# Performance work log

Hardware: AMD Instinct MI355X
Metric: run time of the kernel (lower is better)

## Reference

```python
import jax, jax.numpy as jnp
import numpy as np

C = 512
GROUPS = 32
EPS = 1e-6


def group_norm(x, w, b):
    # x: [B, C, H, W]
    B, Cc, H, W = x.shape
    xg = x.reshape(B, GROUPS, Cc // GROUPS, H, W)
    mean = xg.mean(axis=(2, 3, 4), keepdims=True)
    var = xg.var(axis=(2, 3, 4), keepdims=True)
    xg = (xg - mean) * jax.lax.rsqrt(var + EPS)
    x = xg.reshape(B, Cc, H, W)
    return x * w[None, :, None, None] + b[None, :, None, None]


def conv1x1(x, w, b):
    # 1x1 conv == per-pixel channel matmul; w: [Cout, Cin]
    return jnp.einsum('bchw,oc->bohw', x, w) + b[None, :, None, None]


def setup_inputs() -> dict:
    key = jax.random.key(0)
    ks = jax.random.split(key, 11)
    s = 1.0 / np.sqrt(C)
    d = {
        'x': jax.random.normal(ks[0], (2, C, 64, 64), dtype=jnp.float32),
        'gn_w': jnp.ones((C,), jnp.float32),
        'gn_b': jnp.zeros((C,), jnp.float32),
        'wq': jax.random.normal(ks[1], (C, C), jnp.float32) * s,
        'bq': jax.random.normal(ks[2], (C,), jnp.float32) * 0.01,
        'wk': jax.random.normal(ks[3], (C, C), jnp.float32) * s,
        'bk': jax.random.normal(ks[4], (C,), jnp.float32) * 0.01,
        'wv': jax.random.normal(ks[5], (C, C), jnp.float32) * s,
        'bv': jax.random.normal(ks[6], (C,), jnp.float32) * 0.01,
        'wo': jax.random.normal(ks[7], (C, C), jnp.float32) * s,
        'bo': jax.random.normal(ks[8], (C,), jnp.float32) * 0.01,
    }
    return d


def reference(x, gn_w, gn_b, wq, bq, wk, bk, wv, bv, wo, bo):
    B, Cc, H, W = x.shape
    h = group_norm(x, gn_w, gn_b)
    q = conv1x1(h, wq, bq)  # [B,C,H,W]
    k = conv1x1(h, wk, bk)
    v = conv1x1(h, wv, bv)
    N = H * W
    q = q.reshape(B, Cc, N).transpose(0, 2, 1)   # b n c
    k = k.reshape(B, Cc, N)                      # b c n
    v = v.reshape(B, Cc, N)                      # b c n
    attn = jnp.einsum('bic,bcj->bij', q, k) * (Cc ** -0.5)  # [B,N,N]
    attn = jax.nn.softmax(attn, axis=-1)
    # h_[b,c,i] = sum_j v[b,c,j] * attn[b,i,j]
    h_ = jnp.einsum('bcj,bij->bci', v, attn).reshape(B, Cc, H, W)
    h_ = conv1x1(h_, wo, bo)
    return x + h_
```

## Files before the change

kernel.cpp:

```cpp
#include <hip/hip_runtime.h>


typedef __attribute__((ext_vector_type(8))) short bf16x8;
typedef __attribute__((ext_vector_type(4))) float f32x4;
typedef unsigned short u16;
typedef unsigned int u32;

__device__ __forceinline__ u16 f2bf(float f) {
  u32 u = __builtin_bit_cast(u32, f);
  return (u16)((u + 0x7FFFu + ((u >> 16) & 1u)) >> 16);
}
__device__ __forceinline__ float bf2f(u16 u) {
  return __builtin_bit_cast(float, (u32)u << 16);
}
__device__ __forceinline__ void gll16(const void* g, void* l) {
  __builtin_amdgcn_global_load_lds((const __attribute__((address_space(1))) u32*)g,
                                   (__attribute__((address_space(3))) u32*)l, 16, 0, 0);
}

__global__ __launch_bounds__(256) void gn_stats(const float* __restrict__ x,
                                                float* __restrict__ stats) {
  int bg = blockIdx.x >> 3, slice = blockIdx.x & 7;
  const float4* xp = (const float4*)(x + (size_t)bg * 65536 + slice * 8192);
  int t = threadIdx.x;
  float s = 0.f, ss = 0.f;
  for (int i = t; i < 2048; i += 256) {
    float4 v = xp[i];
    s += v.x + v.y + v.z + v.w;
    ss += v.x * v.x + v.y * v.y + v.z * v.z + v.w * v.w;
  }
  for (int off = 32; off > 0; off >>= 1) {
    s += __shfl_down(s, off);
    ss += __shfl_down(ss, off);
  }
  __shared__ float rs[4], rss[4];
  if ((t & 63) == 0) { rs[t >> 6] = s; rss[t >> 6] = ss; }
  __syncthreads();
  if (t == 0) {
    atomicAdd(&stats[bg * 2 + 0], rs[0] + rs[1] + rs[2] + rs[3]);
    atomicAdd(&stats[bg * 2 + 1], rss[0] + rss[1] + rss[2] + rss[3]);
  }
}

__global__ __launch_bounds__(256) void gn_apply(
    const float* __restrict__ x, const float* __restrict__ w,
    const float* __restrict__ b, const float* __restrict__ stats,
    u16* __restrict__ ht) {
  int bg = blockIdx.x >> 3, slice = blockIdx.x & 7;
  int batch = bg >> 5, g = bg & 31;
  const float* xp = x + (size_t)bg * 65536;
  float mean = stats[bg * 2 + 0] * (1.f / 65536.f);
  float var = stats[bg * 2 + 1] * (1.f / 65536.f) - mean * mean;
  float rstd = rsqrtf(var + 1e-6f);
  float wsc[16], bsc[16];
#pragma unroll
  for (int cc = 0; cc < 16; ++cc) {
    float wv = w[g * 16 + cc];
    wsc[cc] = wv * rstd;
    bsc[cc] = b[g * 16 + cc] - mean * wsc[cc];
  }
  u16* hp = ht + (size_t)batch * 4096 * 512 + g * 16;
  int t = threadIdx.x;
  for (int n = slice * 512 + t; n < slice * 512 + 512; n += 256) {
    union { u16 pk[16]; uint4 v4[2]; } u;
#pragma unroll
    for (int cc = 0; cc < 16; ++cc)
      u.pk[cc] = f2bf(xp[cc * 4096 + n] * wsc[cc] + bsc[cc]);
    uint4* dst = (uint4*)(hp + (size_t)n * 512);
    dst[0] = u.v4[0];
    dst[1] = u.v4[1];
  }
}

__global__ __launch_bounds__(256) void wcvt_kernel(
    const float* __restrict__ wq, const float* __restrict__ wk,
    const float* __restrict__ wv, const float* __restrict__ wo,
    const float* __restrict__ bq, const float* __restrict__ bk,
    u16* __restrict__ Wqk, u16* __restrict__ Wv, u16* __restrict__ Wo,
    float* __restrict__ Bqk, float* __restrict__ stats) {
  int i = blockIdx.x * 256 + threadIdx.x;
  Wqk[i] = f2bf(wq[i]);
  Wqk[262144 + i] = f2bf(wk[i]);
  Wv[i] = f2bf(wv[i]);
  Wo[i] = f2bf(wo[i]);
  if (i < 512) { Bqk[i] = bq[i]; Bqk[512 + i] = bk[i]; }
  if (blockIdx.x == 0 && threadIdx.x < 128) stats[threadIdx.x] = 0.f;
}

template <int BM, int BN, int MODE>
__global__ __launch_bounds__(256) void mfma_gemm(
    const u16* __restrict__ A, int sA, const u16* __restrict__ B, int sB,
    int K, const float* __restrict__ bias, const float* __restrict__ res,
    void* __restrict__ out, int ostr, float scale,
    u16* __restrict__ p1, u16* __restrict__ p2, u16* __restrict__ p3,
    size_t zsA, size_t zsB, size_t zsO) {
  constexpr int TM = BM / 32, TN = BN / 32;
  constexpr int SIA = BM / 32, SIB = BN / 32;
  __shared__ char sm[(BM + BN) * 128];
  char* As = sm;
  char* Bs = sm + BM * 128;
  int t = threadIdx.x;
  int w = t >> 6, lane = t & 63, quad = lane >> 4, ln = lane & 15;
  int wm = w >> 1, wn = w & 1;
  int m0 = blockIdx.y * BM, n0 = blockIdx.x * BN;
  int zb, ksplit;
  if (MODE == 5) { zb = blockIdx.z >> 2; ksplit = blockIdx.z & 3; }
  else           { zb = blockIdx.z;      ksplit = 0; }
  const u16* Ab = A + (size_t)zb * zsA;
  const u16* Bb = B + (size_t)zb * zsB;
  int kbase = ksplit * K;
  f32x4 acc[TM][TN] = {};

  for (int k0 = 0; k0 < K; k0 += 64) {
#pragma unroll
    for (int si = 0; si < SIA; ++si) {
      int s = (w * SIA + si) * 64 + lane;
      gll16(Ab + (size_t)(m0 + (s & (BM - 1))) * sA + kbase + k0 + (s / BM) * 8,
            As + (w * SIA + si) * 1024);
    }
#pragma unroll
    for (int si = 0; si < SIB; ++si) {
      int s = (w * SIB + si) * 64 + lane;
      gll16(Bb + (size_t)(n0 + (s & (BN - 1))) * sB + kbase + k0 + (s / BN) * 8,
            Bs + (w * SIB + si) * 1024);
    }
    __syncthreads();
#pragma unroll
    for (int ks = 0; ks < 2; ++ks) {
      bf16x8 af[TM], bfr[TN];
#pragma unroll
      for (int tm = 0; tm < TM; ++tm)
        af[tm] = *(const bf16x8*)(As + (((ks * 4 + quad) * BM) + wm * (BM / 2) + tm * 16 + ln) * 16);
#pragma unroll
      for (int tn = 0; tn < TN; ++tn)
        bfr[tn] = *(const bf16x8*)(Bs + (((ks * 4 + quad) * BN) + wn * (BN / 2) + tn * 16 + ln) * 16);
#pragma unroll
      for (int tm = 0; tm < TM; ++tm)
#pragma unroll
        for (int tn = 0; tn < TN; ++tn)
          acc[tm][tn] = __builtin_amdgcn_mfma_f32_16x16x32_bf16(af[tm], bfr[tn], acc[tm][tn], 0, 0, 0);
    }
    __syncthreads();
  }

  u16* pdst = nullptr;
  if (MODE == 5) {
    pdst = (ksplit == 0) ? (u16*)out : (ksplit == 1) ? p1
         : (ksplit == 2) ? p2 : p3;
    pdst += (size_t)zb * zsO;
  } else if (MODE != 2) {
    pdst = (u16*)out + (size_t)zb * zsO;
  }

#pragma unroll
  for (int tm = 0; tm < TM; ++tm) {
    int mb = m0 + wm * (BM / 2) + tm * 16 + quad * 4;
#pragma unroll
    for (int tn = 0; tn < TN; ++tn) {
      int n = n0 + wn * (BN / 2) + tn * 16 + ln;
      float bn = (MODE == 0) ? bias[n] : 0.f;
#pragma unroll
      for (int r = 0; r < 4; ++r) {
        int m = mb + r;
        float v = acc[tm][tn][r];
        if (MODE == 0) {
          pdst[(size_t)m * ostr + n] = f2bf(v + bn);
        } else if (MODE == 1) {
          pdst[(size_t)m * ostr + n] = f2bf(v + bias[m]);
        } else if (MODE == 2) {
          int bb = n >> 12, nn = n & 4095;
          size_t off = ((size_t)(bb * 512 + m)) * 4096 + nn;
          ((float*)out)[off] = v + bias[m] + res[off];
        } else if (MODE == 3) {
          pdst[(size_t)m * ostr + n] = f2bf(v * scale);
        } else {
          pdst[(size_t)m * ostr + n] = f2bf(v);
        }
      }
    }
  }
}

__global__ __launch_bounds__(256) void softmax_kernel(u16* __restrict__ S) {
  u16* sp = S + (size_t)blockIdx.x * 4096;
  int t = threadIdx.x;
  int w = t >> 6;
  uint4 a = ((const uint4*)sp)[t * 2];
  uint4 b = ((const uint4*)sp)[t * 2 + 1];
  u32 words[8] = {a.x, a.y, a.z, a.w, b.x, b.y, b.z, b.w};
  float v[16];
#pragma unroll
  for (int i = 0; i < 8; ++i) {
    v[2 * i] = bf2f((u16)(words[i] & 0xFFFF));
    v[2 * i + 1] = bf2f((u16)(words[i] >> 16));
  }
  float mx = v[0];
#pragma unroll
  for (int i = 1; i < 16; ++i) mx = fmaxf(mx, v[i]);
#pragma unroll
  for (int d = 1; d < 64; d <<= 1) mx = fmaxf(mx, __shfl_xor(mx, d));
  __shared__ float red[8];
  if ((t & 63) == 0) red[w] = mx;
  __syncthreads();
  mx = fmaxf(fmaxf(red[0], red[1]), fmaxf(red[2], red[3]));
  float sum = 0.f;
#pragma unroll
  for (int i = 0; i < 16; ++i) {
    v[i] = __expf(v[i] - mx);
    sum += v[i];
  }
#pragma unroll
  for (int d = 1; d < 64; d <<= 1) sum += __shfl_xor(sum, d);
  if ((t & 63) == 0) red[4 + w] = sum;
  __syncthreads();
  float inv = 1.f / (red[4] + red[5] + red[6] + red[7]);
#pragma unroll
  for (int i = 0; i < 8; ++i)
    words[i] = (u32)f2bf(v[2 * i] * inv) | ((u32)f2bf(v[2 * i + 1] * inv) << 16);
  ((uint4*)sp)[t * 2] = make_uint4(words[0], words[1], words[2], words[3]);
  ((uint4*)sp)[t * 2 + 1] = make_uint4(words[4], words[5], words[6], words[7]);
}

__global__ __launch_bounds__(256) void combine4_kernel(
    u16* __restrict__ P0, const u16* __restrict__ P1,
    const u16* __restrict__ P2, const u16* __restrict__ P3) {
  int i = blockIdx.x * 256 + threadIdx.x;
  uint4 a = ((const uint4*)P0)[i];
  uint4 b = ((const uint4*)P1)[i];
  uint4 c = ((const uint4*)P2)[i];
  uint4 d = ((const uint4*)P3)[i];
  u32 wa[4] = {a.x, a.y, a.z, a.w}, wb[4] = {b.x, b.y, b.z, b.w};
  u32 wc[4] = {c.x, c.y, c.z, c.w}, wd[4] = {d.x, d.y, d.z, d.w};
  u32 wo_[4];
#pragma unroll
  for (int q = 0; q < 4; ++q) {
    float lo = bf2f((u16)(wa[q] & 0xFFFF)) + bf2f((u16)(wb[q] & 0xFFFF)) +
               bf2f((u16)(wc[q] & 0xFFFF)) + bf2f((u16)(wd[q] & 0xFFFF));
    float hi = bf2f((u16)(wa[q] >> 16)) + bf2f((u16)(wb[q] >> 16)) +
               bf2f((u16)(wc[q] >> 16)) + bf2f((u16)(wd[q] >> 16));
    wo_[q] = (u32)f2bf(lo) | ((u32)f2bf(hi) << 16);
  }
  ((uint4*)P0)[i] = make_uint4(wo_[0], wo_[1], wo_[2], wo_[3]);
}

extern "C" void kernel_launch(void* const* d_in, const int* in_sizes, int n_in,
                              void* d_out, int out_size, void* d_ws, size_t ws_size,
                              hipStream_t stream) {
  (void)in_sizes; (void)n_in; (void)out_size;
  const float* x = (const float*)d_in[0];
  const float* gnw = (const float*)d_in[1];
  const float* gnb = (const float*)d_in[2];
  const float* wq = (const float*)d_in[3];
  const float* bq = (const float*)d_in[4];
  const float* wk = (const float*)d_in[5];
  const float* bk = (const float*)d_in[6];
  const float* wv = (const float*)d_in[7];
  const float* bv = (const float*)d_in[8];
  const float* wo = (const float*)d_in[9];
  const float* bo = (const float*)d_in[10];
  float* out = (float*)d_out;

  const bool BIG = ws_size >= (size_t)96 * 1024 * 1024;
  char* ws = (char*)d_ws;
  u16* ht  = (u16*)(ws);
  u16* AOt = (u16*)(ws);
  u16* QKt = (u16*)(ws + 8388608);
  u16* S   = (u16*)(ws + 25165824);
  size_t woff = BIG ? 92274688u : 58720256u;
  u16* Wqk = (u16*)(ws + woff);
  u16* Wv  = (u16*)(ws + woff + 1048576);
  u16* Wo  = (u16*)(ws + woff + 1572864);
  float* stats = (float*)(ws + woff + 2097152);
  float* Bqk   = (float*)(ws + woff + 2097664);
  u16* Vg  = (u16*)d_out;
  u16* P1g = (u16*)((char*)d_out + 8388608);

  wcvt_kernel<<<1024, 256, 0, stream>>>(wq, wk, wv, wo, bq, bk, Wqk, Wv, Wo,
                                        Bqk, stats);
  gn_stats<<<512, 256, 0, stream>>>(x, stats);
  gn_apply<<<512, 256, 0, stream>>>(x, gnw, gnb, stats, ht);
  mfma_gemm<128, 128, 0><<<dim3(8, 64), 256, 0, stream>>>(
      ht, 512, Wqk, 512, 512, Bqk, nullptr, QKt, 1024, 1.f,
      nullptr, nullptr, nullptr, 0, 0, 0);
  mfma_gemm<64, 128, 1><<<dim3(64, 8), 256, 0, stream>>>(
      Wv, 512, ht, 512, 512, bv, nullptr, Vg, 8192, 1.f,
      nullptr, nullptr, nullptr, 0, 0, 0);

  if (BIG) {
    mfma_gemm<128, 128, 3><<<dim3(32, 32, 2), 256, 0, stream>>>(
        QKt, 1024, QKt + 512, 1024, 512, nullptr, nullptr, S, 4096,
        0.044194173824159216f, nullptr, nullptr, nullptr,
        4194304u, 4194304u, 16777216u);
    softmax_kernel<<<8192, 256, 0, stream>>>(S);
    mfma_gemm<128, 128, 5><<<dim3(4, 32, 8), 256, 0, stream>>>(
        S, 4096, Vg, 8192, 1024, nullptr, nullptr,
        AOt, 512, 1.f, P1g, QKt, QKt + 4194304, 16777216u, 4096u, 2097152u);
    combine4_kernel<<<2048, 256, 0, stream>>>(AOt, P1g, QKt, QKt + 4194304);
  } else {
    u16* P2g = (u16*)((char*)d_out + 12582912);
    for (int b = 0; b < 2; ++b) {
      const u16* Qb = QKt + (size_t)b * 4194304;
      mfma_gemm<128, 128, 3><<<dim3(32, 32), 256, 0, stream>>>(
          Qb, 1024, Qb + 512, 1024, 512, nullptr, nullptr, S, 4096,
          0.044194173824159216f, nullptr, nullptr, nullptr, 0, 0, 0);
      softmax_kernel<<<4096, 256, 0, stream>>>(S);
      u16* P0 = AOt + (size_t)b * 2097152;
      u16* P3 = QKt + (size_t)b * 4194304;
      mfma_gemm<128, 128, 5><<<dim3(4, 32, 4), 256, 0, stream>>>(
          S, 4096, Vg + (size_t)b * 4096, 8192, 1024, nullptr, nullptr,
          P0, 512, 1.f, P1g, P2g, P3, 0, 0, 0);
      combine4_kernel<<<1024, 256, 0, stream>>>(P0, P1g, P2g, P3);
    }
  }
  mfma_gemm<64, 128, 2><<<dim3(64, 8), 256, 0, stream>>>(
      Wo, 512, AOt, 512, 512, bo, x, out, 0, 1.f,
      nullptr, nullptr, nullptr, 0, 0, 0);
}
```

Baseline: 364.8 us.

## Fuse softmax exp into QK GEMM epilogue and defer normalization to combine

The QK^T GEMM epilogue now writes exp(scaled score) directly and atomically accumulates per-row sums, removing the separate softmax kernel pass over the large score matrix. Normalization by the row sum is deferred to the split-K combine kernel. This skips max subtraction, so it relies on scores staying small enough not to overflow exp, and it adds atomic traffic. It applies only on the large-workspace path.

```diff
diff --git a/kernel.cpp b/kernel.cpp
--- a/kernel.cpp
+++ b/kernel.cpp
@@ -77,14 +77,16 @@
     const float* __restrict__ wv, const float* __restrict__ wo,
     const float* __restrict__ bq, const float* __restrict__ bk,
     u16* __restrict__ Wqk, u16* __restrict__ Wv, u16* __restrict__ Wo,
-    float* __restrict__ Bqk, float* __restrict__ stats) {
+    float* __restrict__ Bqk, float* __restrict__ stats,
+    float* __restrict__ lsum) {
   int i = blockIdx.x * 256 + threadIdx.x;
   Wqk[i] = f2bf(wq[i]);
   Wqk[262144 + i] = f2bf(wk[i]);
   Wv[i] = f2bf(wv[i]);
   Wo[i] = f2bf(wo[i]);
   if (i < 512) { Bqk[i] = bq[i]; Bqk[512 + i] = bk[i]; }
-  if (blockIdx.x == 0 && threadIdx.x < 128) stats[threadIdx.x] = 0.f;
+  if (i < 128) stats[i] = 0.f;
+  if (i < 8192) lsum[i] = 0.f;
 }
 
 template <int BM, int BN, int MODE>
@@ -93,7 +95,7 @@
     int K, const float* __restrict__ bias, const float* __restrict__ res,
     void* __restrict__ out, int ostr, float scale,
     u16* __restrict__ p1, u16* __restrict__ p2, u16* __restrict__ p3,
-    size_t zsA, size_t zsB, size_t zsO) {
+    size_t zsA, size_t zsB, size_t zsO, float* __restrict__ lsum) {
   constexpr int TM = BM / 32, TN = BN / 32;
   constexpr int SIA = BM / 32, SIB = BN / 32;
   __shared__ char sm[(BM + BN) * 128];
@@ -150,6 +152,28 @@
     pdst += (size_t)zb * zsO;
   } else if (MODE != 2) {
     pdst = (u16*)out + (size_t)zb * zsO;
+  }
+
+  if (MODE == 6) {
+#pragma unroll
+    for (int tm = 0; tm < TM; ++tm) {
+#pragma unroll
+      for (int r = 0; r < 4; ++r) {
+        int m = m0 + wm * (BM / 2) + tm * 16 + quad * 4 + r;
+        float rsum = 0.f;
+#pragma unroll
+        for (int tn = 0; tn < TN; ++tn) {
+          int n = n0 + wn * (BN / 2) + tn * 16 + ln;
+          float e = __expf(acc[tm][tn][r] * scale);
+          rsum += e;
+          pdst[(size_t)m * ostr + n] = f2bf(e);
+        }
+#pragma unroll
+        for (int d = 1; d < 16; d <<= 1) rsum += __shfl_xor(rsum, d);
+        if (ln == 0) atomicAdd(&lsum[(size_t)zb * 4096 + m], rsum);
+      }
+    }
+    return;
   }
 
 #pragma unroll
@@ -221,10 +245,13 @@
   ((uint4*)sp)[t * 2 + 1] = make_uint4(words[4], words[5], words[6], words[7]);
 }
 
+template <bool NORM>
 __global__ __launch_bounds__(256) void combine4_kernel(
     u16* __restrict__ P0, const u16* __restrict__ P1,
-    const u16* __restrict__ P2, const u16* __restrict__ P3) {
+    const u16* __restrict__ P2, const u16* __restrict__ P3,
+    const float* __restrict__ lsum) {
   int i = blockIdx.x * 256 + threadIdx.x;
+  float inv = NORM ? 1.f / lsum[i >> 6] : 1.f;
   uint4 a = ((const uint4*)P0)[i];
   uint4 b = ((const uint4*)P1)[i];
   uint4 c = ((const uint4*)P2)[i];
@@ -238,7 +265,7 @@
                bf2f((u16)(wc[q] & 0xFFFF)) + bf2f((u16)(wd[q] & 0xFFFF));
     float hi = bf2f((u16)(wa[q] >> 16)) + bf2f((u16)(wb[q] >> 16)) +
                bf2f((u16)(wc[q] >> 16)) + bf2f((u16)(wd[q] >> 16));
-    wo_[q] = (u32)f2bf(lo) | ((u32)f2bf(hi) << 16);
+    wo_[q] = (u32)f2bf(lo * inv) | ((u32)f2bf(hi * inv) << 16);
   }
   ((uint4*)P0)[i] = make_uint4(wo_[0], wo_[1], wo_[2], wo_[3]);
 }
@@ -272,47 +299,50 @@
   u16* Wo  = (u16*)(ws + woff + 1572864);
   float* stats = (float*)(ws + woff + 2097152);
   float* Bqk   = (float*)(ws + woff + 2097664);
+  float* lsum  = (float*)(ws + woff + 2101760);
   u16* Vg  = (u16*)d_out;
   u16* P1g = (u16*)((char*)d_out + 8388608);
 
   wcvt_kernel<<<1024, 256, 0, stream>>>(wq, wk, wv, wo, bq, bk, Wqk, Wv, Wo,
-                                        Bqk, stats);
+                                        Bqk, stats, lsum);
   gn_stats<<<512, 256, 0, stream>>>(x, stats);
   gn_apply<<<512, 256, 0, stream>>>(x, gnw, gnb, stats, ht);
   mfma_gemm<128, 128, 0><<<dim3(8, 64), 256, 0, stream>>>(
       ht, 512, Wqk, 512, 512, Bqk, nullptr, QKt, 1024, 1.f,
-      nullptr, nullptr, nullptr, 0, 0, 0);
+      nullptr, nullptr, nullptr, 0, 0, 0, nullptr);
   mfma_gemm<64, 128, 1><<<dim3(64, 8), 256, 0, stream>>>(
       Wv, 512, ht, 512, 512, bv, nullptr, Vg, 8192, 1.f,
-      nullptr, nullptr, nullptr, 0, 0, 0);
+      nullptr, nullptr, nullptr, 0, 0, 0, nullptr);
 
   if (BIG) {
-    mfma_gemm<128, 128, 3><<<dim3(32, 32, 2), 256, 0, stream>>>(
+    mfma_gemm<128, 128, 6><<<dim3(32, 32, 2), 256, 0, stream>>>(
         QKt, 1024, QKt + 512, 1024, 512, nullptr, nullptr, S, 4096,
         0.044194173824159216f, nullptr, nullptr, nullptr,
-        4194304u, 4194304u, 16777216u);
-    softmax_kernel<<<8192, 256, 0, stream>>>(S);
+        4194304u, 4194304u, 16777216u, lsum);
     mfma_gemm<128, 128, 5><<<dim3(4, 32, 8), 256, 0, stream>>>(
         S, 4096, Vg, 8192, 1024, nullptr, nullptr,
-        AOt, 512, 1.f, P1g, QKt, QKt + 4194304, 16777216u, 4096u, 2097152u);
-    combine4_kernel<<<2048, 256, 0, stream>>>(AOt, P1g, QKt, QKt + 4194304);
+        AOt, 512, 1.f, P1g, QKt, QKt + 4194304, 16777216u, 4096u, 2097152u,
+        nullptr);
+    combine4_kernel<true><<<2048, 256, 0, stream>>>(
+        AOt, P1g, QKt, QKt + 4194304, lsum);
   } else {
     u16* P2g = (u16*)((char*)d_out + 12582912);
     for (int b = 0; b < 2; ++b) {
       const u16* Qb = QKt + (size_t)b * 4194304;
       mfma_gemm<128, 128, 3><<<dim3(32, 32), 256, 0, stream>>>(
           Qb, 1024, Qb + 512, 1024, 512, nullptr, nullptr, S, 4096,
-          0.044194173824159216f, nullptr, nullptr, nullptr, 0, 0, 0);
+          0.044194173824159216f, nullptr, nullptr, nullptr, 0, 0, 0, nullptr);
       softmax_kernel<<<4096, 256, 0, stream>>>(S);
       u16* P0 = AOt + (size_t)b * 2097152;
       u16* P3 = QKt + (size_t)b * 4194304;
       mfma_gemm<128, 128, 5><<<dim3(4, 32, 4), 256, 0, stream>>>(
           S, 4096, Vg + (size_t)b * 4096, 8192, 1024, nullptr, nullptr,
-          P0, 512, 1.f, P1g, P2g, P3, 0, 0, 0);
-      combine4_kernel<<<1024, 256, 0, stream>>>(P0, P1g, P2g, P3);
+          P0, 512, 1.f, P1g, P2g, P3, 0, 0, 0, nullptr);
+      combine4_kernel<false><<<1024, 256, 0, stream>>>(P0, P1g, P2g, P3,
+                                                       nullptr);
     }
   }
   mfma_gemm<64, 128, 2><<<dim3(64, 8), 256, 0, stream>>>(
       Wo, 512, AOt, 512, 512, bo, x, out, 0, 1.f,
-      nullptr, nullptr, nullptr, 0, 0, 0);
-}
+      nullptr, nullptr, nullptr, 0, 0, 0, nullptr);
+}
```

New measurement: 360.8 us. Within noise of the previous version (-1.1%).
